# Kernel optimization log

Hardware: AMD Instinct MI355X
Metric: run time of the kernel (lower is better)

Reference implementation:

```python
import jax, jax.numpy as jnp
import numpy as np
from jax import lax

S = 16  # encoder stride (patchify-conv stand-in for the CNN backbone, stride-16 feature grid)


def _conv(x, w, b, stride, padding):
    y = lax.conv_general_dilated(x, w, (stride, stride), padding,
                                 dimension_numbers=('NCHW', 'OIHW', 'NCHW'))
    return y + b[None, :, None, None]


def _l2norm(x, eps=1e-12):  # F.normalize(p=2, dim=1)
    n = jnp.sqrt(jnp.sum(x * x, axis=1, keepdims=True))
    return x / jnp.maximum(n, eps)


def _encode(frame, ew, eb, kw, kb, vw, vb, mask=None):
    feat = jax.nn.relu(_conv(frame, ew, eb, S, 'VALID'))  # [B,512,h,w]
    key = _conv(feat, kw, kb, 1, 'SAME')                  # [B,64,h,w]
    val = _conv(feat, vw, vb, 1, 'SAME')                  # [B,ed,h,w]
    if mask is not None:
        m = mask[:, None, ::S, ::S]  # torch F.interpolate 'nearest' with exact integer factor
        key = key * m
        val = val * m
    return _l2norm(key), val, feat


def _forward(query_frame, prev_frame, prev_mask, first_frame, first_mask,
             enc_q_w, enc_q_b, enc_m_w, enc_m_b,
             key_w, key_b, val_w, val_b,
             dec1_w, dec1_b, dec2_w, dec2_b, cls_w, cls_b):
    # memory bank reset + push(first), push(prev)
    k1, v1, _ = _encode(first_frame, enc_m_w, enc_m_b, key_w, key_b, val_w, val_b, first_mask)
    kp, vp, _ = _encode(prev_frame, enc_m_w, enc_m_b, key_w, key_b, val_w, val_b, prev_mask)
    qk, qv, _ = _encode(query_frame, enc_q_w, enc_q_b, key_w, key_b, val_w, val_b)
    B, Ck, h, w = qk.shape
    ed = qv.shape[1]
    mem_key = jnp.concatenate([k1.reshape(B, Ck, -1), kp.reshape(B, Ck, -1)], axis=2)  # [B,64,M]
    mem_val = jnp.concatenate([v1.reshape(B, ed, -1), vp.reshape(B, ed, -1)], axis=2)  # [B,ed,M]
    q_key = qk.reshape(B, Ck, -1)                                                      # [B,64,Q]
    # STM memory read: affinity -> softmax -> weighted sum over memory pixels
    affinity = jnp.einsum('bcq,bcm->bqm', q_key, mem_key) / jnp.sqrt(jnp.float32(Ck))
    affinity = jax.nn.softmax(affinity, axis=-1)
    mem_read = jnp.einsum('bqm,bcm->bcq', affinity, mem_val).reshape(B, ed, h, w)
    fused = jnp.concatenate([qv, mem_read], axis=1)  # [B,2*ed,h,w] (aspp=False)
    d = jax.nn.relu(_conv(fused, dec1_w, dec1_b, 1, 'SAME'))
    dec_feat = jax.nn.relu(_conv(d, dec2_w, dec2_b, 1, 'SAME'))
    logits = _conv(dec_feat, cls_w, cls_b, 1, 'SAME')
    H, W = query_frame.shape[-2], query_frame.shape[-1]
    logits_full = jax.image.resize(logits, (B, logits.shape[1], H, W), method='bilinear')  # align_corners=False
    rep_feat = _l2norm(dec_feat)
    return rep_feat, logits_full


def setup_inputs():
    key = jax.random.key(0)
    ks = jax.random.split(key, 16)
    B, H, W = 8, 512, 512
    Ce, Ck, ed = 512, 64, 256
    g = lambda i, sh, s: jax.random.normal(ks[i], sh, dtype=jnp.float32) * s
    return {
        'query_frame': g(0, (B, 3, H, W), 1.0),
        'prev_frame': g(1, (B, 3, H, W), 1.0),
        'prev_mask': jnp.round(jax.random.uniform(ks[2], (B, H, W), dtype=jnp.float32)),
        'first_frame': g(3, (B, 3, H, W), 1.0),
        'first_mask': jnp.round(jax.random.uniform(ks[4], (B, H, W), dtype=jnp.float32)),
        'enc_q_w': g(5, (Ce, 3, S, S), 0.02), 'enc_q_b': jnp.zeros((Ce,), jnp.float32),
        'enc_m_w': g(6, (Ce, 3, S, S), 0.02), 'enc_m_b': jnp.zeros((Ce,), jnp.float32),
        'key_w': g(7, (Ck, Ce, 1, 1), 0.05), 'key_b': jnp.zeros((Ck,), jnp.float32),
        'val_w': g(8, (ed, Ce, 1, 1), 0.05), 'val_b': jnp.zeros((ed,), jnp.float32),
        'dec1_w': g(9, (ed, 2 * ed, 3, 3), 0.02), 'dec1_b': jnp.zeros((ed,), jnp.float32),
        'dec2_w': g(10, (ed, ed, 3, 3), 0.02), 'dec2_b': jnp.zeros((ed,), jnp.float32),
        'cls_w': g(11, (2, ed, 1, 1), 0.05), 'cls_b': jnp.zeros((2,), jnp.float32),
    }


def reference(query_frame, prev_frame, prev_mask, first_frame, first_mask,
              enc_q_w, enc_q_b, enc_m_w, enc_m_b,
              key_w, key_b, val_w, val_b,
              dec1_w, dec1_b, dec2_w, dec2_b, cls_w, cls_b):
    return _forward(query_frame, prev_frame, prev_mask, first_frame, first_mask,
                    enc_q_w, enc_q_b, enc_m_w, enc_m_b,
                    key_w, key_b, val_w, val_b,
                    dec1_w, dec1_b, dec2_w, dec2_b, cls_w, cls_b)
```

## Files before the change

kernel.cpp:

```cpp
#include <hip/hip_runtime.h>
#include <hip/hip_bf16.h>
#include <cstdint>

#define DEV __device__ __forceinline__
typedef __attribute__((ext_vector_type(8))) short short8;
typedef __attribute__((ext_vector_type(4))) float f32x4;
typedef unsigned short u16;

DEV float b2f(u16 u) { union { unsigned int i; float f; } x; x.i = (unsigned)u << 16; return x.f; }
DEV u16 f2b(float f) { __hip_bfloat16 h = __float2bfloat16(f); return *(u16*)&h; }
DEV float rdin(const void* p, size_t i, int isbf) {
  return isbf ? __bfloat162float(((const __hip_bfloat16*)p)[i]) : ((const float*)p)[i];
}
DEV void wrout(void* p, size_t i, float v, int isbf) {
  if (isbf) ((__hip_bfloat16*)p)[i] = __float2bfloat16(v);
  else      ((float*)p)[i] = v;
}
DEV short8 ld8(const void* p, size_t idx, int isbf) {
  if (isbf) return *(const short8*)((const u16*)p + idx);
  const float* f = (const float*)p + idx;
  float4 x = *(const float4*)f, y = *(const float4*)(f + 4);
  short8 r;
  r[0] = f2b(x.x); r[1] = f2b(x.y); r[2] = f2b(x.z); r[3] = f2b(x.w);
  r[4] = f2b(y.x); r[5] = f2b(y.y); r[6] = f2b(y.z); r[7] = f2b(y.w);
  return r;
}
DEV void gl16(const u16* g, u16* l) {
  __builtin_amdgcn_global_load_lds(
      (const __attribute__((address_space(1))) void*)g,
      (__attribute__((address_space(3))) void*)l, 16, 0, 0);
}
DEV void bar() {
  asm volatile("" ::: "memory");
  __builtin_amdgcn_s_barrier();
  asm volatile("" ::: "memory");
}

__global__ __launch_bounds__(256) void detect_k(const u16* w, int* flag) {
  __shared__ int cnt[256];
  int tid = threadIdx.x, c = 0;
  for (int i = tid; i < 4096; i += 256) {
    u16 v = w[i];
    int e = (v >> 7) & 0xFF;
    if (v == 0 || (e >= 0x60 && e <= 0x9F)) c++;
  }
  cnt[tid] = c;
  __syncthreads();
  for (int s = 128; s > 0; s >>= 1) { if (tid < s) cnt[tid] += cnt[tid + s]; __syncthreads(); }
  if (tid == 0) *flag = (cnt[0] > 3600) ? 1 : 0;
}

__global__ __launch_bounds__(256) void patchify_k(const void* F0, const void* F1,
                                                  u16* dst, const int* dflag) {
  int isbf = *dflag;
  int bid = blockIdx.x;
  int z = bid >> 8, rem = bid & 255, b = rem >> 5, y = rem & 31;
  const void* F = z ? F1 : F0;
  int x = threadIdx.x & 31, pj = threadIdx.x >> 5;
  u16* drow = dst + (size_t)(z * 8192 + b * 1024 + y * 32 + x) * 768;
#pragma unroll
  for (int i = 0; i < 6; i++) {
    int pair = i * 8 + pj;
    int c = pair >> 4, ky = pair & 15;
    size_t src = ((size_t)((b * 3 + c) * 512 + y * 16 + ky)) * 512 + x * 16;
    short8 v0 = ld8(F, src, isbf);
    short8 v1 = ld8(F, src + 8, isbf);
    u16* dp = drow + c * 256 + ky * 16;
    *(short8*)dp = v0;
    *(short8*)(dp + 8) = v1;
  }
}

__global__ __launch_bounds__(256) void wconv_k(const void* wm, const void* wq,
                                               u16* dst, const int* dflag) {
  int isbf = *dflag;
  int gi = blockIdx.x * 256 + threadIdx.x;
  size_t e0 = (size_t)gi * 8;
  const void* src = e0 < 393216 ? wm : wq;
  size_t off = e0 < 393216 ? e0 : e0 - 393216;
  *(short8*)&dst[e0] = ld8(src, off, isbf);
}

__global__ __launch_bounds__(256) void kvconv_k(const void* valW, const void* keyW,
                                                u16* dst, const int* dflag) {
  int isbf = *dflag;
  int idx = blockIdx.x * 256 + threadIdx.x;
  size_t e0 = (size_t)idx * 8;
  int row = (int)(e0 >> 9);
  const void* src = row < 256 ? valW : keyW;
  size_t off = row < 256 ? e0 : e0 - (size_t)256 * 512;
  *(short8*)&dst[e0] = ld8(src, off, isbf);
}

struct PA {
  const void* W0; const void* W1; size_t bs; int K; int rowsplit; int zsel; int ws16; int rowmax1;
  DEV short8 l8(int row, int k, int b, int zz, int isbf) const {
    const void* W = W0; int r = row;
    if (zsel && zz == 2) W = W1;
    else if (rowsplit && row >= rowsplit) { W = W1; r = row - rowsplit; if (r > rowmax1) r = rowmax1; }
    return ld8(W, (size_t)b * bs + (size_t)r * K + k, ws16 ? 1 : isbf);
  }
  DEV const u16* ga(int row, int k, int b, int zz) const {
    int r = row; if (rowsplit && r > rowmax1) r = rowmax1;
    return (const u16*)W0 + (size_t)b * bs + (size_t)r * K + k;
  }
};
struct PBws {
  const u16* X; int rs; size_t zs;
  DEV short8 l8(int t, int k, int zz, int) const {
    return *(const short8*)(X + (size_t)zz * zs + (size_t)t * rs + k);
  }
  DEV const u16* ga(int t, int k, int zz) const {
    return X + (size_t)zz * zs + (size_t)t * rs + k;
  }
};
struct PBc3 {
  const u16* X; int C; int shift;
  DEV short8 l8(int t, int k, int, int) const {
    int tap = k >> shift, c0 = k & (C - 1);
    int dy = tap / 3, dx = tap - dy * 3;
    int pos = t & 1023, y = pos >> 5, x = pos & 31;
    int iy = y + dy - 1, ix = x + dx - 1;
    if ((unsigned)iy >= 32u || (unsigned)ix >= 32u) { short8 z = {0,0,0,0,0,0,0,0}; return z; }
    return *(const short8*)(X + (size_t)(((t >> 10) * 1024) + iy * 32 + ix) * C + c0);
  }
};

struct Epi {
  int mode;
  u16 *o16, *o16b, *o16c;
  size_t zs; int ts, moff, mmax;
  const void *bias, *bias2; int bzsel;
  const void *maskA, *maskB;
  const float* rscale;
  float scale; int relu, doexp;
  DEV void store1(int m, int t, int z, float v, int isbf) const {
    if (m >= mmax) return;
    int b = t >> 10, pos = t & 1023;
    if (m < 256) {
      v += rdin(bias, m, isbf);
      if (z < 2) {
        const void* mk = z ? maskB : maskA;
        v *= rdin(mk, ((size_t)(b * 512 + (pos >> 5) * 16) << 9) + (pos & 31) * 16, isbf);
        o16[((size_t)(b * 256 + m)) * 2048 + (size_t)z * 1024 + pos] = f2b(v);
      } else {
        o16b[(size_t)t * 512 + m] = f2b(v);
      }
    } else {
      v += rdin(bias2, m - 256, isbf);
      o16c[((size_t)z * 8192 + t) * 64 + (m - 256)] = f2b(v);
    }
  }
};

DEV void epilogue(const Epi& ep, f32x4 (&acc)[4][4], u16* sh, int isbf, int tid,
                  int col16, int quad, int wm, int wn, int zz, int m0, int n0, int nbase) {
  if (ep.mode == 1) {
#pragma unroll
    for (int mt = 0; mt < 4; mt++)
#pragma unroll
      for (int nt = 0; nt < 4; nt++)
#pragma unroll
        for (int r = 0; r < 4; r++) {
          int m = m0 + wm * 64 + mt * 16 + quad * 4 + r;
          int t = nbase + n0 + wn * 64 + nt * 16 + col16;
          ep.store1(m, t, zz, acc[mt][nt][r], isbf);
        }
    return;
  }
  if (ep.mode == 2) {
    float* pf = (float*)ep.o16;
#pragma unroll
    for (int mt = 0; mt < 4; mt++)
#pragma unroll
      for (int nt = 0; nt < 4; nt++)
#pragma unroll
        for (int r = 0; r < 4; r++) {
          int m = m0 + wm * 64 + mt * 16 + quad * 4 + r;
          int t = nbase + n0 + wn * 64 + nt * 16 + col16;
          pf[((size_t)(zz * 256 + m)) * 8192 + t] = acc[mt][nt][r];
        }
    return;
  }
  u16* T = sh;
  const int TS = 132;
  for (int p = 0; p < 2; p++) {
    __syncthreads();
    if (wn == p) {
#pragma unroll
      for (int mt = 0; mt < 4; mt++)
#pragma unroll
        for (int nt = 0; nt < 4; nt++) {
          int tl = nt * 16 + col16;
#pragma unroll
          for (int r2 = 0; r2 < 2; r2++) {
            int ml = wm * 64 + mt * 16 + quad * 4 + r2 * 2;
            float v0 = acc[mt][nt][r2 * 2] * ep.scale;
            float v1 = acc[mt][nt][r2 * 2 + 1] * ep.scale;
            if (ep.bias) {
              const void* bp = (ep.bzsel && zz == 2) ? ep.bias2 : ep.bias;
              v0 += rdin(bp, m0 + ml, isbf);
              v1 += rdin(bp, m0 + ml + 1, isbf);
            }
            if (ep.relu) { v0 = fmaxf(v0, 0.f); v1 = fmaxf(v1, 0.f); }
            unsigned int pk = (unsigned)f2b(v0) | ((unsigned)f2b(v1) << 16);
            *(unsigned int*)&T[tl * TS + ml] = pk;
          }
        }
    }
    __syncthreads();
    {
      int tl = tid >> 2, seg = tid & 3;
      int tg = nbase + n0 + p * 64 + tl;
      u16* op = ep.o16 + (size_t)zz * ep.zs + (size_t)tg * ep.ts + ep.moff + m0;
#pragma unroll
      for (int i = 0; i < 4; i++) {
        int c8 = seg + i * 4;
        short8 v = *(short8*)&T[tl * TS + c8 * 8];
        *(short8*)&op[c8 * 8] = v;
      }
    }
  }
}

template <class PB>
__global__ __launch_bounds__(256) void mgl(PA pa, PB pb, Epi ep, int ktiles, int nbase,
                                           const int* dflag) {
  __shared__ u16 sh[32768];
  int isbf = *dflag;
  int tid = threadIdx.x, lane = tid & 63;
  int col16 = lane & 15, quad = lane >> 4;
  int wv = tid >> 6, wm = wv >> 1, wn = wv & 1;
  int zz = blockIdx.z;
  int n0 = blockIdx.x * 128, m0 = blockIdx.y * 128;
  int bA = (nbase + n0) >> 10;

  f32x4 acc[4][4];
#pragma unroll
  for (int mt = 0; mt < 4; mt++)
#pragma unroll
    for (int nt = 0; nt < 4; nt++)
#pragma unroll
      for (int r = 0; r < 4; r++) acc[mt][nt][r] = 0.f;

  int rA[4], lA[4];
#pragma unroll
  for (int g = 0; g < 4; g++) {
    rA[g] = g * 32 + (tid >> 3);
    lA[g] = (tid & 7) ^ (rA[g] & 7);
  }

  auto issue = [&](int kt) {
    int kk = kt * 64;
    u16* base = sh + ((kt & 1) << 14);
#pragma unroll
    for (int g = 0; g < 4; g++) {
      gl16(pa.ga(m0 + rA[g], kk + lA[g] * 8, bA, zz), base + (size_t)(g * 256 + tid) * 8);
      gl16(pb.ga(nbase + n0 + rA[g], kk + lA[g] * 8, zz), base + 8192 + (size_t)(g * 256 + tid) * 8);
    }
  };
  issue(0);

  for (int kt = 0; kt < ktiles; kt++) {
    const u16* As = sh + ((kt & 1) << 14);
    const u16* Bs = As + 8192;
    if (kt + 1 < ktiles) {
      issue(kt + 1);
      asm volatile("s_waitcnt vmcnt(8)" ::: "memory");
    } else {
      asm volatile("s_waitcnt vmcnt(0)" ::: "memory");
    }
    bar();
#pragma unroll
    for (int s = 0; s < 2; s++) {
      short8 af[4], bf[4];
      int cs = ((s * 4 + quad) ^ (col16 & 7)) << 3;
#pragma unroll
      for (int mt = 0; mt < 4; mt++)
        af[mt] = *(const short8*)&As[(wm * 64 + mt * 16 + col16) * 64 + cs];
#pragma unroll
      for (int nt = 0; nt < 4; nt++)
        bf[nt] = *(const short8*)&Bs[(wn * 64 + nt * 16 + col16) * 64 + cs];
#pragma unroll
      for (int mt = 0; mt < 4; mt++)
#pragma unroll
        for (int nt = 0; nt < 4; nt++)
          acc[mt][nt] = __builtin_amdgcn_mfma_f32_16x16x32_bf16(af[mt], bf[nt], acc[mt][nt], 0, 0, 0);
    }
    bar();
  }

  epilogue(ep, acc, sh, isbf, tid, col16, quad, wm, wn, zz, m0, n0, nbase);
}

template <class PB>
__global__ __launch_bounds__(256) void mg(PA pa, PB pb, Epi ep, int ktiles, int nbase,
                                          int ksplit, const int* dflag) {
  __shared__ u16 sh[32768];
  int isbf = *dflag;
  int tid = threadIdx.x, lane = tid & 63;
  int col16 = lane & 15, quad = lane >> 4;
  int wv = tid >> 6, wm = wv >> 1, wn = wv & 1;
  int zz = blockIdx.z;
  int kb = ksplit * zz;
  int n0 = blockIdx.x * 128, m0 = blockIdx.y * 128;
  int bA = (nbase + n0) >> 10;

  f32x4 acc[4][4];
#pragma unroll
  for (int mt = 0; mt < 4; mt++)
#pragma unroll
    for (int nt = 0; nt < 4; nt++)
#pragma unroll
      for (int r = 0; r < 4; r++) acc[mt][nt][r] = 0.f;

  int rA[4], lA[4];
#pragma unroll
  for (int g = 0; g < 4; g++) {
    rA[g] = g * 32 + (tid >> 3);
    lA[g] = (tid & 7) ^ (rA[g] & 7);
  }

  short8 ra[4], rb[4];
#pragma unroll
  for (int g = 0; g < 4; g++) {
    ra[g] = pa.l8(m0 + rA[g], kb + lA[g] * 8, bA, zz, isbf);
    rb[g] = pb.l8(nbase + n0 + rA[g], kb + lA[g] * 8, zz, isbf);
  }
#pragma unroll
  for (int g = 0; g < 4; g++) {
    *(short8*)&sh[(size_t)(g * 256 + tid) * 8] = ra[g];
    *(short8*)&sh[8192 + (size_t)(g * 256 + tid) * 8] = rb[g];
  }
  __syncthreads();

  for (int kt = 0; kt < ktiles; kt++) {
    const u16* As = sh + ((kt & 1) ? 16384 : 0);
    const u16* Bs = As + 8192;
    bool more = (kt + 1 < ktiles);
    if (more) {
      int kn = kb + (kt + 1) * 64;
#pragma unroll
      for (int g = 0; g < 4; g++) {
        ra[g] = pa.l8(m0 + rA[g], kn + lA[g] * 8, bA, zz, isbf);
        rb[g] = pb.l8(nbase + n0 + rA[g], kn + lA[g] * 8, zz, isbf);
      }
    }
#pragma unroll
    for (int s = 0; s < 2; s++) {
      short8 af[4], bf[4];
      int cs = ((s * 4 + quad) ^ (col16 & 7)) << 3;
#pragma unroll
      for (int mt = 0; mt < 4; mt++)
        af[mt] = *(const short8*)&As[(wm * 64 + mt * 16 + col16) * 64 + cs];
#pragma unroll
      for (int nt = 0; nt < 4; nt++)
        bf[nt] = *(const short8*)&Bs[(wn * 64 + nt * 16 + col16) * 64 + cs];
#pragma unroll
      for (int mt = 0; mt < 4; mt++)
#pragma unroll
        for (int nt = 0; nt < 4; nt++)
          acc[mt][nt] = __builtin_amdgcn_mfma_f32_16x16x32_bf16(af[mt], bf[nt], acc[mt][nt], 0, 0, 0);
    }
    if (more) {
      u16* An = sh + (!(kt & 1) ? 16384 : 0);
#pragma unroll
      for (int g = 0; g < 4; g++) {
        *(short8*)&An[(size_t)(g * 256 + tid) * 8] = ra[g];
        *(short8*)&An[8192 + (size_t)(g * 256 + tid) * 8] = rb[g];
      }
      __syncthreads();
    }
  }

  epilogue(ep, acc, sh, isbf, tid, col16, quad, wm, wn, zz, m0, n0, nbase);
}

__global__ __launch_bounds__(256) void attn_k(const u16* qk, const u16* memk,
                                              const u16* memv, float* pf, float* rsum) {
  __shared__ u16 sh[28672];
  __shared__ float rsl[64];
  const int Qt = 0, Kt = 4096, Vt = 8192, Pl = 24576;
  int tid = threadIdx.x, lane = tid & 63;
  int col16 = lane & 15, quad = lane >> 4;
  int wv = tid >> 6;
  int b = blockIdx.x >> 4, qt = blockIdx.x & 15;
  int q0 = b * 1024 + qt * 64;
  int s = blockIdx.y;
  int kv0 = s * 512;

  if (tid < 64) rsl[tid] = 0.f;

  int r32 = tid >> 3;
#pragma unroll
  for (int g = 0; g < 2; g++) {
    int row = g * 32 + r32;
    int k8 = (tid & 7) ^ (row & 7);
    gl16(qk + (size_t)(q0 + row) * 64 + k8 * 8, sh + Qt + (size_t)(g * 256 + tid) * 8);
  }
  {
#pragma unroll
    for (int g = 0; g < 2; g++) {
      int row = g * 32 + r32;
      int k8 = (tid & 7) ^ (row & 7);
      gl16(memk + ((size_t)(b * 2048 + kv0 + row)) * 64 + k8 * 8,
           sh + Kt + (size_t)(g * 256 + tid) * 8);
    }
#pragma unroll
    for (int g = 0; g < 8; g++) {
      int row = g * 32 + r32;
      int k8 = (tid & 7) ^ (row & 7);
      gl16(memv + ((size_t)(b * 256 + row)) * 2048 + kv0 + k8 * 8,
           sh + Vt + (size_t)(g * 256 + tid) * 8);
    }
  }
  __syncthreads();

  f32x4 acc_o[4][4];
#pragma unroll
  for (int mt = 0; mt < 4; mt++)
#pragma unroll
    for (int nt = 0; nt < 4; nt++)
#pragma unroll
      for (int r = 0; r < 4; r++) acc_o[mt][nt][r] = 0.f;

  for (int ch = 0; ch < 8; ch++) {
    if (tid < 64) {
      f32x4 acc_s[4][4];
#pragma unroll
      for (int mt = 0; mt < 4; mt++)
#pragma unroll
        for (int nt = 0; nt < 4; nt++)
#pragma unroll
          for (int r = 0; r < 4; r++) acc_s[mt][nt][r] = 0.f;
#pragma unroll
      for (int s2 = 0; s2 < 2; s2++) {
        short8 af[4], bf[4];
        int cs = ((s2 * 4 + quad) ^ (col16 & 7)) << 3;
#pragma unroll
        for (int mt = 0; mt < 4; mt++)
          af[mt] = *(const short8*)&sh[Kt + (mt * 16 + col16) * 64 + cs];
#pragma unroll
        for (int nt = 0; nt < 4; nt++)
          bf[nt] = *(const short8*)&sh[Qt + (nt * 16 + col16) * 64 + cs];
#pragma unroll
        for (int mt = 0; mt < 4; mt++)
#pragma unroll
          for (int nt = 0; nt < 4; nt++)
            acc_s[mt][nt] = __builtin_amdgcn_mfma_f32_16x16x32_bf16(af[mt], bf[nt], acc_s[mt][nt], 0, 0, 0);
      }
#pragma unroll
      for (int nt = 0; nt < 4; nt++) {
        int ql = nt * 16 + col16;
        float tsum = 0.f;
#pragma unroll
        for (int mt = 0; mt < 4; mt++)
#pragma unroll
          for (int r = 0; r < 4; r++) {
            int kvl = mt * 16 + quad * 4 + r;
            u16 pb = f2b(__expf(0.125f * acc_s[mt][nt][r]));
            tsum += b2f(pb);
            sh[Pl + ql * 64 + (((kvl >> 3) ^ (ql & 7)) << 3) + (kvl & 7)] = pb;
          }
        tsum += __shfl_xor(tsum, 16);
        tsum += __shfl_xor(tsum, 32);
        if (quad == 0) rsl[ql] += tsum;
      }
    }
    __syncthreads();
#pragma unroll
    for (int s2 = 0; s2 < 2; s2++) {
      short8 af[4], bf[4];
      int cs = ((s2 * 4 + quad) ^ (col16 & 7)) << 3;
#pragma unroll
      for (int mt = 0; mt < 4; mt++)
        af[mt] = *(const short8*)&sh[Vt + (wv * 64 + mt * 16 + col16) * 64 + cs];
#pragma unroll
      for (int nt = 0; nt < 4; nt++)
        bf[nt] = *(const short8*)&sh[Pl + (nt * 16 + col16) * 64 + cs];
#pragma unroll
      for (int mt = 0; mt < 4; mt++)
#pragma unroll
        for (int nt = 0; nt < 4; nt++)
          acc_o[mt][nt] = __builtin_amdgcn_mfma_f32_16x16x32_bf16(af[mt], bf[nt], acc_o[mt][nt], 0, 0, 0);
    }
    __syncthreads();
    if (ch + 1 < 8) {
      int kvc = kv0 + (ch + 1) * 64;
#pragma unroll
      for (int g = 0; g < 2; g++) {
        int row = g * 32 + r32;
        int k8 = (tid & 7) ^ (row & 7);
        gl16(memk + ((size_t)(b * 2048 + kvc + row)) * 64 + k8 * 8,
             sh + Kt + (size_t)(g * 256 + tid) * 8);
      }
#pragma unroll
      for (int g = 0; g < 8; g++) {
        int row = g * 32 + r32;
        int k8 = (tid & 7) ^ (row & 7);
        gl16(memv + ((size_t)(b * 256 + row)) * 2048 + kvc + k8 * 8,
             sh + Vt + (size_t)(g * 256 + tid) * 8);
      }
    }
    __syncthreads();
  }

#pragma unroll
  for (int mt = 0; mt < 4; mt++)
#pragma unroll
    for (int nt = 0; nt < 4; nt++)
#pragma unroll
      for (int r = 0; r < 4; r++) {
        int c = wv * 64 + mt * 16 + quad * 4 + r;
        int q = nt * 16 + col16;
        pf[((size_t)(s * 8192 + q0 + q)) * 256 + c] = acc_o[mt][nt][r];
      }
  if (tid < 64) atomicAdd(&rsum[q0 + tid], rsl[tid]);
}

__global__ __launch_bounds__(256) void acomb_k(const float* pf, const float* rsum,
                                               u16* fused) {
  int tid = threadIdx.x;
  int t = blockIdx.x * 2 + (tid >> 7);
  int cp = tid & 127;
  float inv = 1.f / rsum[t];
  float v0 = 0.f, v1 = 0.f;
#pragma unroll
  for (int s = 0; s < 4; s++) {
    const float* p = pf + ((size_t)(s * 8192 + t)) * 256 + cp * 2;
    v0 += p[0]; v1 += p[1];
  }
  unsigned int pk = (unsigned)f2b(v0 * inv) | ((unsigned)f2b(v1 * inv) << 16);
  *(unsigned int*)&fused[(size_t)t * 512 + 256 + cp * 2] = pk;
}

__global__ __launch_bounds__(256) void comb_k(const float* pf, const void* bias,
                                              u16* out, int ts, int moff, int npart,
                                              int relu, const int* dflag) {
  int isbf = *dflag;
  int tid = threadIdx.x;
  int t = blockIdx.x * 64 + (tid & 63);
  int m = blockIdx.y * 8 + ((tid >> 6) << 1);
  float v0 = 0.f, v1 = 0.f;
  for (int p = 0; p < npart; p++) {
    v0 += pf[(size_t)(p * 256 + m) * 8192 + t];
    v1 += pf[(size_t)(p * 256 + m + 1) * 8192 + t];
  }
  if (bias) { v0 += rdin(bias, m, isbf); v1 += rdin(bias, m + 1, isbf); }
  if (relu) { v0 = fmaxf(v0, 0.f); v1 = fmaxf(v1, 0.f); }
  unsigned int pk = (unsigned)f2b(v0) | ((unsigned)f2b(v1) << 16);
  *(unsigned int*)&out[(size_t)t * ts + moff + m] = pk;
}

__global__ __launch_bounds__(256) void wreorder_k(const void* src, u16* dst, int C,
                                                  int total, const int* dflag) {
  int idx = blockIdx.x * 256 + threadIdx.x;
  if (idx >= total) return;
  int isbf = *dflag;
  int nine_c = 9 * C;
  int m = idx / nine_c; int r = idx - m * nine_c;
  int tp = r / C; int c = r - tp * C;
  dst[idx] = f2b(rdin(src, (size_t)(m * C + c) * 9 + tp, isbf));
}

__global__ __launch_bounds__(256) void keyfix_k(const u16* kraw3, const void* mA,
                                                const void* mB, u16* memk, u16* qk,
                                                float* rsum, const int* dflag) {
  int isbf = *dflag;
  int z = blockIdx.y;
  int n = blockIdx.x * 256 + threadIdx.x;
  int b = n >> 10, pos = n & 1023;
  if (z == 0) rsum[n] = 0.f;
  float mv = 1.f;
  if (z == 0) mv = rdin(mA, ((size_t)(b * 512 + (pos >> 5) * 16) << 9) + (pos & 31) * 16, isbf);
  else if (z == 1) mv = rdin(mB, ((size_t)(b * 512 + (pos >> 5) * 16) << 9) + (pos & 31) * 16, isbf);
  const u16* src = kraw3 + ((size_t)z * 8192 + n) * 64;
  float v[64], ss = 0.f;
#pragma unroll
  for (int c = 0; c < 64; c++) { v[c] = b2f(src[c]) * mv; ss += v[c] * v[c]; }
  float inv = 1.f / fmaxf(sqrtf(ss), 1e-12f);
  u16* dst = (z < 2) ? memk + (size_t)(b * 2048 + z * 1024 + pos) * 64 : qk + (size_t)n * 64;
#pragma unroll
  for (int c = 0; c < 64; c++) dst[c] = f2b(v[c] * inv);
}

__global__ __launch_bounds__(256) void repcls_k(const u16* decf, const void* cwgt,
                                                const void* cbias, void* out_rep,
                                                float* logits, const int* dflag) {
  int isbf = *dflag;
  int tid = threadIdx.x, lane = tid & 63, wv = tid >> 6;
  int tok = blockIdx.x * 4 + wv;
  int b = tok >> 10, pos = tok & 1023;
  const u16* src = decf + (size_t)tok * 256;
  int c0 = lane * 4;
  float v[4], ss = 0.f, a0 = 0.f, a1 = 0.f;
#pragma unroll
  for (int j = 0; j < 4; j++) {
    float x = b2f(src[c0 + j]);
    v[j] = x; ss += x * x;
    a0 = fmaf(x, rdin(cwgt, c0 + j, isbf), a0);
    a1 = fmaf(x, rdin(cwgt, 256 + c0 + j, isbf), a1);
  }
#pragma unroll
  for (int off = 32; off > 0; off >>= 1) {
    ss += __shfl_down(ss, off); a0 += __shfl_down(a0, off); a1 += __shfl_down(a1, off);
  }
  ss = __shfl(ss, 0); a0 = __shfl(a0, 0); a1 = __shfl(a1, 0);
  float inv = 1.f / fmaxf(sqrtf(ss), 1e-12f);
#pragma unroll
  for (int j = 0; j < 4; j++)
    wrout(out_rep, ((size_t)(b * 256 + c0 + j) << 10) + pos, v[j] * inv, isbf);
  if (lane == 0) {
    logits[((size_t)(b * 2) << 10) + pos]     = a0 + rdin(cbias, 0, isbf);
    logits[((size_t)(b * 2 + 1) << 10) + pos] = a1 + rdin(cbias, 1, isbf);
  }
}

__global__ __launch_bounds__(256) void resize_k(const float* logits, void* out,
                                                size_t ebase, const int* dflag) {
  int isbf = *dflag;
  int idx = blockIdx.x * 256 + threadIdx.x;
  int ox = idx & 511, oy = (idx >> 9) & 511, c = (idx >> 18) & 1, b = idx >> 19;
  float fy = (oy + 0.5f) * 0.0625f - 0.5f;
  float fx = (ox + 0.5f) * 0.0625f - 0.5f;
  int y0 = (int)floorf(fy), x0 = (int)floorf(fx);
  float wy = fy - y0, wx = fx - x0;
  int y0c = max(y0, 0), y1c = min(y0 + 1, 31);
  int x0c = max(x0, 0), x1c = min(x0 + 1, 31);
  const float* L = logits + ((size_t)(b * 2 + c) << 10);
  float v00 = L[y0c * 32 + x0c], v01 = L[y0c * 32 + x1c];
  float v10 = L[y1c * 32 + x0c], v11 = L[y1c * 32 + x1c];
  float v = (1.f - wy) * ((1.f - wx) * v00 + wx * v01) + wy * ((1.f - wx) * v10 + wx * v11);
  wrout(out, ebase + (size_t)idx, v, isbf);
}

extern "C" void kernel_launch(void* const* d_in, const int* in_sizes, int n_in,
                              void* d_out, int out_size, void* d_ws, size_t ws_size,
                              hipStream_t stream) {
  const void* query  = d_in[0];  const void* prev   = d_in[1];
  const void* prevM  = d_in[2];  const void* first  = d_in[3];
  const void* firstM = d_in[4];  const void* encQw  = d_in[5];
  const void* encQb  = d_in[6];  const void* encMw  = d_in[7];
  const void* encMb  = d_in[8];  const void* keyW   = d_in[9];
  const void* keyB   = d_in[10]; const void* valW   = d_in[11];
  const void* valB   = d_in[12]; const void* dec1W  = d_in[13];
  const void* dec1B  = d_in[14]; const void* dec2W  = d_in[15];
  const void* dec2B  = d_in[16]; const void* clsW   = d_in[17];
  const void* clsB   = d_in[18];

  u16* W = (u16*)d_ws;
  int* dflag = (int*)W;
  float* rsum   = (float*)(W + 16);
  float* logits = (float*)(W + 16400);
  u16* B0 = W + 49168;
  u16* Xp    = B0;
  u16* feat3 = B0 + 12582912;
  u16* encWb = B0 + 25165824;
  u16* wr1   = B0;
  u16* wr2   = B0 + 1179648;
  u16* fused = B0 + 1769472;
  u16* memv  = B0 + 5963776;
  u16* memk  = B0 + 10158080;
  u16* qk    = B0 + 11206656;
  u16* kraw3 = B0 + 25165824;
  u16* kvW   = B0 + 26738688;
  float* pf  = (float*)(B0 + 11730944);
  u16* dbuf  = memv;
  u16* decf  = memv + 2097152;

  dim3 blk(256);
  detect_k<<<dim3(1), blk, 0, stream>>>((const u16*)encQw, dflag);

  wconv_k<<<dim3(384), blk, 0, stream>>>(encMw, encQw, encWb, dflag);
  patchify_k<<<dim3(512), blk, 0, stream>>>(first, prev, Xp, dflag);
  {
    PA a{encWb, 0, 0, 768, 0, 0, 1, 0};
    PBws b{Xp, 768, (size_t)8192 * 768};
    Epi e{0, feat3, 0, 0, (size_t)8192 * 512, 512, 0, 512,
          encMb, 0, 0, 0, 0, 0, 1.f, 1, 0};
    mgl<PBws><<<dim3(64, 4, 2), blk, 0, stream>>>(a, b, e, 12, 0, dflag);
  }
  patchify_k<<<dim3(256), blk, 0, stream>>>(query, query, Xp, dflag);
  {
    PA a{encWb + 393216, 0, 0, 768, 0, 0, 1, 0};
    PBws b{Xp, 768, 0};
    Epi e{0, feat3 + (size_t)2 * 8192 * 512, 0, 0, 0, 512, 0, 512,
          encQb, 0, 0, 0, 0, 0, 1.f, 1, 0};
    mgl<PBws><<<dim3(64, 4, 1), blk, 0, stream>>>(a, b, e, 12, 0, dflag);
  }

  wreorder_k<<<dim3(4608), blk, 0, stream>>>(dec1W, wr1, 512, 256 * 4608, dflag);
  wreorder_k<<<dim3(2304), blk, 0, stream>>>(dec2W, wr2, 256, 256 * 2304, dflag);
  kvconv_k<<<dim3(80), blk, 0, stream>>>(valW, keyW, kvW, dflag);

  {
    PA a{kvW, 0, 0, 512, 1, 0, 1, 319};
    PBws b{feat3, 512, (size_t)8192 * 512};
    Epi e{1, memv, fused, kraw3, 0, 0, 0, 320,
          valB, keyB, 0, firstM, prevM, 0, 1.f, 0, 0};
    mgl<PBws><<<dim3(64, 3, 3), blk, 0, stream>>>(a, b, e, 8, 0, dflag);
  }
  keyfix_k<<<dim3(32, 3), blk, 0, stream>>>(kraw3, firstM, prevM, memk, qk, rsum, dflag);

  attn_k<<<dim3(128, 4), blk, 0, stream>>>(qk, memk, memv, pf, rsum);
  acomb_k<<<dim3(4096), blk, 0, stream>>>(pf, rsum, fused);

  {
    PA a{wr1, 0, 0, 4608, 0, 0, 1, 0};
    PBc3 b{fused, 512, 9};
    Epi e{2, (u16*)pf, 0, 0, 0, 0, 0, 0,
          0, 0, 0, 0, 0, 0, 1.f, 0, 0};
    mg<PBc3><<<dim3(64, 2, 4), blk, 0, stream>>>(a, b, e, 18, 0, 1152, dflag);
    comb_k<<<dim3(128, 32), blk, 0, stream>>>(pf, dec1B, dbuf, 256, 0, 4, 1, dflag);
  }
  {
    PA a{wr2, 0, 0, 2304, 0, 0, 1, 0};
    PBc3 b{dbuf, 256, 8};
    Epi e{2, (u16*)pf, 0, 0, 0, 0, 0, 0,
          0, 0, 0, 0, 0, 0, 1.f, 0, 0};
    mg<PBc3><<<dim3(64, 2, 2), blk, 0, stream>>>(a, b, e, 18, 0, 1152, dflag);
    comb_k<<<dim3(128, 32), blk, 0, stream>>>(pf, dec2B, decf, 256, 0, 2, 1, dflag);
  }

  repcls_k<<<dim3(2048), blk, 0, stream>>>(decf, clsW, clsB, d_out, logits, dflag);
  resize_k<<<dim3(16384), blk, 0, stream>>>(logits, d_out, (size_t)2097152, dflag);
}
```

Measured before the change: 471.4 us.

## Split attention score computation across all four waves and overlap K prefetch

The QK^T score and exp stage, previously done only by wave 0 while the other three waves idled, is now split so each wave computes a 16-row slice of the key chunk, with per-wave row-sum partials reduced at the end. The next K chunk load is issued before the PV MFMA step so it overlaps that compute, with V reloaded after a barrier. Block indices are also remapped to interleave batches and query tiles across the grid. The aim is to remove the serial single-wave bottleneck in the softmax stage, at the cost of extra shared-memory partial sums and a reordered barrier structure.

```diff
diff --git a/kernel.cpp b/kernel.cpp
--- a/kernel.cpp
+++ b/kernel.cpp
@@ -379,17 +379,19 @@
 __global__ __launch_bounds__(256) void attn_k(const u16* qk, const u16* memk,
                                               const u16* memv, float* pf, float* rsum) {
   __shared__ u16 sh[28672];
-  __shared__ float rsl[64];
+  __shared__ float rsl[4][64];
   const int Qt = 0, Kt = 4096, Vt = 8192, Pl = 24576;
   int tid = threadIdx.x, lane = tid & 63;
   int col16 = lane & 15, quad = lane >> 4;
   int wv = tid >> 6;
-  int b = blockIdx.x >> 4, qt = blockIdx.x & 15;
+  int xl = blockIdx.x;
+  int x = ((xl & 7) << 4) | (xl >> 3);
+  int b = x >> 4, qt = x & 15;
   int q0 = b * 1024 + qt * 64;
   int s = blockIdx.y;
   int kv0 = s * 512;
 
-  if (tid < 64) rsl[tid] = 0.f;
+  rsl[wv][lane] = 0.f;
 
   int r32 = tid >> 3;
 #pragma unroll
@@ -425,64 +427,39 @@
       for (int r = 0; r < 4; r++) acc_o[mt][nt][r] = 0.f;
 
   for (int ch = 0; ch < 8; ch++) {
-    if (tid < 64) {
-      f32x4 acc_s[4][4];
-#pragma unroll
-      for (int mt = 0; mt < 4; mt++)
-#pragma unroll
-        for (int nt = 0; nt < 4; nt++)
-#pragma unroll
-          for (int r = 0; r < 4; r++) acc_s[mt][nt][r] = 0.f;
+    {
+      f32x4 acc_s[4];
+#pragma unroll
+      for (int nt = 0; nt < 4; nt++)
+#pragma unroll
+        for (int r = 0; r < 4; r++) acc_s[nt][r] = 0.f;
 #pragma unroll
       for (int s2 = 0; s2 < 2; s2++) {
-        short8 af[4], bf[4];
         int cs = ((s2 * 4 + quad) ^ (col16 & 7)) << 3;
-#pragma unroll
-        for (int mt = 0; mt < 4; mt++)
-          af[mt] = *(const short8*)&sh[Kt + (mt * 16 + col16) * 64 + cs];
+        short8 af = *(const short8*)&sh[Kt + (wv * 16 + col16) * 64 + cs];
+        short8 bf[4];
 #pragma unroll
         for (int nt = 0; nt < 4; nt++)
           bf[nt] = *(const short8*)&sh[Qt + (nt * 16 + col16) * 64 + cs];
 #pragma unroll
-        for (int mt = 0; mt < 4; mt++)
-#pragma unroll
-          for (int nt = 0; nt < 4; nt++)
-            acc_s[mt][nt] = __builtin_amdgcn_mfma_f32_16x16x32_bf16(af[mt], bf[nt], acc_s[mt][nt], 0, 0, 0);
+        for (int nt = 0; nt < 4; nt++)
+          acc_s[nt] = __builtin_amdgcn_mfma_f32_16x16x32_bf16(af, bf[nt], acc_s[nt], 0, 0, 0);
       }
 #pragma unroll
       for (int nt = 0; nt < 4; nt++) {
         int ql = nt * 16 + col16;
         float tsum = 0.f;
 #pragma unroll
-        for (int mt = 0; mt < 4; mt++)
-#pragma unroll
-          for (int r = 0; r < 4; r++) {
-            int kvl = mt * 16 + quad * 4 + r;
-            u16 pb = f2b(__expf(0.125f * acc_s[mt][nt][r]));
-            tsum += b2f(pb);
-            sh[Pl + ql * 64 + (((kvl >> 3) ^ (ql & 7)) << 3) + (kvl & 7)] = pb;
-          }
+        for (int r = 0; r < 4; r++) {
+          int kvl = wv * 16 + quad * 4 + r;
+          u16 pb = f2b(__expf(0.125f * acc_s[nt][r]));
+          tsum += b2f(pb);
+          sh[Pl + ql * 64 + (((kvl >> 3) ^ (ql & 7)) << 3) + (kvl & 7)] = pb;
+        }
         tsum += __shfl_xor(tsum, 16);
         tsum += __shfl_xor(tsum, 32);
-        if (quad == 0) rsl[ql] += tsum;
-      }
-    }
-    __syncthreads();
-#pragma unroll
-    for (int s2 = 0; s2 < 2; s2++) {
-      short8 af[4], bf[4];
-      int cs = ((s2 * 4 + quad) ^ (col16 & 7)) << 3;
-#pragma unroll
-      for (int mt = 0; mt < 4; mt++)
-        af[mt] = *(const short8*)&sh[Vt + (wv * 64 + mt * 16 + col16) * 64 + cs];
-#pragma unroll
-      for (int nt = 0; nt < 4; nt++)
-        bf[nt] = *(const short8*)&sh[Pl + (nt * 16 + col16) * 64 + cs];
-#pragma unroll
-      for (int mt = 0; mt < 4; mt++)
-#pragma unroll
-        for (int nt = 0; nt < 4; nt++)
-          acc_o[mt][nt] = __builtin_amdgcn_mfma_f32_16x16x32_bf16(af[mt], bf[nt], acc_o[mt][nt], 0, 0, 0);
+        if (quad == 0) rsl[wv][ql] += tsum;
+      }
     }
     __syncthreads();
     if (ch + 1 < 8) {
@@ -494,6 +471,26 @@
         gl16(memk + ((size_t)(b * 2048 + kvc + row)) * 64 + k8 * 8,
              sh + Kt + (size_t)(g * 256 + tid) * 8);
       }
+    }
+#pragma unroll
+    for (int s2 = 0; s2 < 2; s2++) {
+      short8 af[4], bf[4];
+      int cs = ((s2 * 4 + quad) ^ (col16 & 7)) << 3;
+#pragma unroll
+      for (int mt = 0; mt < 4; mt++)
+        af[mt] = *(const short8*)&sh[Vt + (wv * 64 + mt * 16 + col16) * 64 + cs];
+#pragma unroll
+      for (int nt = 0; nt < 4; nt++)
+        bf[nt] = *(const short8*)&sh[Pl + (nt * 16 + col16) * 64 + cs];
+#pragma unroll
+      for (int mt = 0; mt < 4; mt++)
+#pragma unroll
+        for (int nt = 0; nt < 4; nt++)
+          acc_o[mt][nt] = __builtin_amdgcn_mfma_f32_16x16x32_bf16(af[mt], bf[nt], acc_o[mt][nt], 0, 0, 0);
+    }
+    __syncthreads();
+    if (ch + 1 < 8) {
+      int kvc = kv0 + (ch + 1) * 64;
 #pragma unroll
       for (int g = 0; g < 8; g++) {
         int row = g * 32 + r32;
@@ -515,7 +512,8 @@
         int q = nt * 16 + col16;
         pf[((size_t)(s * 8192 + q0 + q)) * 256 + c] = acc_o[mt][nt][r];
       }
-  if (tid < 64) atomicAdd(&rsum[q0 + tid], rsl[tid]);
+  if (tid < 64)
+    atomicAdd(&rsum[q0 + tid], rsl[0][tid] + rsl[1][tid] + rsl[2][tid] + rsl[3][tid]);
 }
 
 __global__ __launch_bounds__(256) void acomb_k(const float* pf, const float* rsum,
```

After: 441.8 us. 6.3% less time.
